# Optimization experiments

Measured on AMD Instinct MI355X. Metric: run time of the kernel, lower is better.

The kernel has to match this reference:

```python
import jax, jax.numpy as jnp
import numpy as np

B, H, W, D, C = 2, 16, 16, 16, 128
UNITS = 128
BN_EPS = 1e-3  # keras BatchNormalization default epsilon


def setup_inputs() -> dict:
    key = jax.random.key(0)
    ks = jax.random.split(key, 12)
    lim = np.sqrt(3.0 / C)  # VarianceScaling(1.0, fan_avg, uniform)
    inp = {
        "x": jax.random.normal(ks[0], (B, H, W, D, C), dtype=jnp.float32),
        "gamma": jnp.ones((C,), jnp.float32),
        "beta": jnp.zeros((C,), jnp.float32),
        "moving_mean": jax.random.normal(ks[1], (C,), jnp.float32) * 0.1,
        "moving_var": jnp.ones((C,), jnp.float32) + 0.1 * jax.random.uniform(ks[2], (C,)),
        "Wq": jax.random.uniform(ks[3], (C, UNITS), jnp.float32, -lim, lim),
        "bq": jnp.zeros((UNITS,), jnp.float32),
        "Wk": jax.random.uniform(ks[4], (C, UNITS), jnp.float32, -lim, lim),
        "bk": jnp.zeros((UNITS,), jnp.float32),
        "Wv": jax.random.uniform(ks[5], (C, UNITS), jnp.float32, -lim, lim),
        "bv": jnp.zeros((UNITS,), jnp.float32),
        # proj uses kernel_init(0.0) -> effectively ~0; use tiny scale to keep grads nonzero
        "Wp": jax.random.uniform(ks[6], (UNITS, UNITS), jnp.float32, -1e-5, 1e-5),
        "bp": jnp.zeros((UNITS,), jnp.float32),
    }
    return inp


def reference(x, gamma, beta, moving_mean, moving_var, Wq, bq, Wk, bk, Wv, bv, Wp, bp):
    # BatchNormalization (inference mode): per-channel affine normalization
    xn = (x - moving_mean) * jax.lax.rsqrt(moving_var + BN_EPS) * gamma + beta
    b, h, w, d, c = xn.shape
    n = h * w * d
    scale = jnp.asarray(UNITS, jnp.float32) ** -0.5
    q = (xn @ Wq + bq).reshape(b, n, UNITS)
    k = (xn @ Wk + bk).reshape(b, n, UNITS)
    v = (xn @ Wv + bv).reshape(b, n, UNITS)
    # full self-attention over flattened 3D spatial dims: [b, n, n] scores
    attn = jax.nn.softmax(jnp.einsum('bnc,bmc->bnm', q, k) * scale, axis=-1)
    proj = jnp.einsum('bnm,bmc->bnc', attn, v).reshape(b, h, w, d, UNITS)
    proj = proj @ Wp + bp
    return xn + proj
```

## Files before the change

kernel.cpp:

```cpp
#include <hip/hip_runtime.h>
#include <hip/hip_bf16.h>

using bh8     = __attribute__((ext_vector_type(8))) short;
using floatx4 = __attribute__((ext_vector_type(4))) float;
using uintx2  = __attribute__((ext_vector_type(2))) unsigned;

#define MFMA16 __builtin_amdgcn_mfma_f32_16x16x32_bf16

__device__ __forceinline__ float b2f(short s) {
    union { unsigned u; float f; } v; v.u = ((unsigned)(unsigned short)s) << 16; return v.f;
}
__device__ __forceinline__ short f2b(float f) {
    union { float f; unsigned u; } v; v.f = f;
    unsigned r = (v.u + 0x7fffu + ((v.u >> 16) & 1u)) >> 16;
    return (short)r;
}
__device__ __forceinline__ unsigned pk2(float a, float b) {
    union { __hip_bfloat162 h; unsigned u; } v;
    v.h = __float22bfloat162_rn(make_float2(a, b));
    return v.u;
}
__device__ __forceinline__ float ldf(const void* p, int i, bool f32) {
    return f32 ? ((const float*)p)[i] : b2f(((const short*)p)[i]);
}
__device__ __forceinline__ bool detect_f32(const void* gamma) {
    return ((*(const unsigned*)gamma) & 0xFFFFu) == 0u;
}
__device__ __forceinline__ void gl2lds16(const short* g, short* l) {
    __builtin_amdgcn_global_load_lds(
        (const __attribute__((address_space(1))) void*)g,
        (__attribute__((address_space(3))) void*)l, 16, 0, 0);
}

#define WAITV(N) do { asm volatile("s_waitcnt vmcnt(" #N ")" ::: "memory"); \
                      __builtin_amdgcn_sched_barrier(0); } while (0)

#define LDW 136

__global__ __launch_bounds__(256) void k_bn_qkv(
    const void* __restrict__ xp,
    const void* __restrict__ gp, const void* __restrict__ bep,
    const void* __restrict__ mmp, const void* __restrict__ mvp,
    const void* __restrict__ Wqp, const void* __restrict__ bqp,
    const void* __restrict__ Wkp, const void* __restrict__ bkp,
    const void* __restrict__ Wvp, const void* __restrict__ bvp,
    short* __restrict__ Qo, short* __restrict__ Ko, short* __restrict__ Vt)
{
    __shared__ float sS[128], sT[128];
    __shared__ __align__(16) short Wt[128 * LDW];
    const bool f32 = detect_f32(gp);
    const int tid = threadIdx.x, wave = tid >> 6, lane = tid & 63;
    const int lq = lane >> 4, lr = lane & 15;
    const int g = blockIdx.x >> 6;
    const int tile = blockIdx.x & 63;
    const int row0 = tile * 128 + wave * 32;

    if (tid < 128) {
        float ga = ldf(gp, tid, f32), be = ldf(bep, tid, f32);
        float mm = ldf(mmp, tid, f32), mv = ldf(mvp, tid, f32);
        float s = ga * rsqrtf(mv + 1e-3f);
        sS[tid] = s;
        sT[tid] = be - mm * s;
    }

    const void* W  = (g == 0) ? Wqp : ((g == 1) ? Wkp : Wvp);
    const void* bb = (g == 0) ? bqp : ((g == 1) ? bkp : bvp);

    if (f32) {
        for (int it = 0; it < 16; ++it) {
            int f = (it * 256 + tid) * 4;
            int c = f >> 7, u = f & 127;
            floatx4 wv = *(const floatx4*)((const float*)W + f);
            #pragma unroll
            for (int jj = 0; jj < 4; ++jj) {
                int j = (jj + (tid >> 1)) & 3;
                Wt[(u + j) * LDW + c] = f2b(wv[j]);
            }
        }
    } else {
        for (int it = 0; it < 8; ++it) {
            int f = (it * 256 + tid) * 8;
            int c = f >> 7, u = f & 127;
            bh8 wv = *(const bh8*)((const short*)W + f);
            #pragma unroll
            for (int jj = 0; jj < 8; ++jj) {
                int j = (jj + tid) & 7;
                Wt[(u + j) * LDW + c] = wv[j];
            }
        }
    }
    __syncthreads();

    bh8 a[2][4];
    #pragma unroll
    for (int rt = 0; rt < 2; ++rt)
        #pragma unroll
        for (int ks = 0; ks < 4; ++ks) {
            int c0 = ks * 32 + lq * 8;
            floatx4 s0 = *(const floatx4*)(&sS[c0]), s1 = *(const floatx4*)(&sS[c0 + 4]);
            floatx4 t0 = *(const floatx4*)(&sT[c0]), t1 = *(const floatx4*)(&sT[c0 + 4]);
            bh8 af;
            if (f32) {
                const float* xr = (const float*)xp + (size_t)(row0 + rt * 16 + lr) * 128 + c0;
                floatx4 x0 = *(const floatx4*)xr, x1 = *(const floatx4*)(xr + 4);
                #pragma unroll
                for (int j = 0; j < 4; ++j) {
                    af[j]     = f2b(x0[j] * s0[j] + t0[j]);
                    af[j + 4] = f2b(x1[j] * s1[j] + t1[j]);
                }
            } else {
                bh8 xv = *(const bh8*)((const short*)xp + (size_t)(row0 + rt * 16 + lr) * 128 + c0);
                #pragma unroll
                for (int j = 0; j < 4; ++j) {
                    af[j]     = f2b(b2f(xv[j]) * s0[j] + t0[j]);
                    af[j + 4] = f2b(b2f(xv[j + 4]) * s1[j] + t1[j]);
                }
            }
            a[rt][ks] = af;
        }

    floatx4 acc[2][8] = {};
    #pragma unroll
    for (int ks = 0; ks < 4; ++ks)
        #pragma unroll
        for (int t = 0; t < 8; ++t) {
            bh8 b = *(const bh8*)(&Wt[(t * 16 + lr) * LDW + ks * 32 + lq * 8]);
            #pragma unroll
            for (int rt = 0; rt < 2; ++rt)
                acc[rt][t] = MFMA16(a[rt][ks], b, acc[rt][t], 0, 0, 0);
        }

    if (g < 2) {
        #pragma unroll
        for (int t = 0; t < 8; ++t) {
            int u = t * 16 + lr;
            float bias = ldf(bb, u, f32);
            #pragma unroll
            for (int rt = 0; rt < 2; ++rt)
                #pragma unroll
                for (int r = 0; r < 4; ++r) {
                    int grow = row0 + rt * 16 + lq * 4 + r;
                    short vb = f2b(acc[rt][t][r] + bias);
                    if (g == 0) Qo[(size_t)grow * 128 + u] = vb;
                    else        Ko[(size_t)grow * 128 + u] = vb;
                }
        }
    } else {
        __syncthreads();
        short* sVt = Wt;
        #pragma unroll
        for (int t = 0; t < 8; ++t) {
            int u = t * 16 + lr;
            float bias = ldf(bb, u, f32);
            #pragma unroll
            for (int rt = 0; rt < 2; ++rt)
                #pragma unroll
                for (int r = 0; r < 4; ++r) {
                    int n = wave * 32 + rt * 16 + lq * 4 + r;
                    sVt[u * LDW + n] = f2b(acc[rt][t][r] + bias);
                }
        }
        __syncthreads();
        int u = tid >> 1, nh = tid & 1;
        int grow0 = tile * 128 + nh * 64;
        int bsb = grow0 >> 12, nn = grow0 & 4095;
        short* dst = Vt + (size_t)bsb * 128 * 4096 + (size_t)u * 4096 + nn;
        #pragma unroll
        for (int j = 0; j < 8; ++j)
            *(bh8*)(dst + j * 8) = *(const bh8*)(&sVt[u * LDW + nh * 64 + j * 8]);
    }
}

#define PLDA 40

__global__ __launch_bounds__(256, 2) void k_attn(
    const short* __restrict__ Qg, const short* __restrict__ Kg,
    const short* __restrict__ Vtg, short* __restrict__ Op,
    float* __restrict__ Lq)
{
    __shared__ __align__(16) short sK[4][32 * 128];
    __shared__ __align__(16) short sV[4][128 * 32];
    __shared__ __align__(16) short sP[4][32 * PLDA];

    const int tid = threadIdx.x, wave = tid >> 6, lane = tid & 63;
    const int lq = lane >> 4, lr = lane & 15;
    const int qt = blockIdx.x >> 3, kq = blockIdx.x & 7;
    const int mq = qt * 128, bs = mq >> 12, key0q = kq * 512;
    const short* Kb = Kg + (size_t)bs * 4096 * 128;
    const short* Vb = Vtg + (size_t)bs * 128 * 4096;
    const int qrow0 = mq + wave * 32;

    bh8 aq[2][4];
    #pragma unroll
    for (int rt = 0; rt < 2; ++rt)
        #pragma unroll
        for (int ks = 0; ks < 4; ++ks)
            aq[rt][ks] = *(const bh8*)(Qg + (size_t)(qrow0 + rt * 16 + lr) * 128 + ks * 32 + lq * 8);

    const int kKey = lane >> 4, kCh = lane & 15;
    const int vU   = lane >> 2, vCh = lane & 3;

    floatx4 accO[2][8] = {};
    float lsum[2] = {};
    const float c2 = 0.12751743f;
    const float m2 = 11.541560f;
    short* Pw = &sP[wave][0];

    auto stage = [&](int tt, int bb) {
        const int key1 = key0q + tt * 32;
        #pragma unroll
        for (int rd = 0; rd < 2; ++rd) {
            int key = wave * 8 + rd * 4 + kKey;
            gl2lds16(Kb + (size_t)(key1 + key) * 128 + ((kCh ^ (key & 7)) << 3),
                     &sK[bb][(wave * 8 + rd * 4) * 128]);
        }
        #pragma unroll
        for (int rd = 0; rd < 2; ++rd) {
            int u = wave * 32 + rd * 16 + vU;
            gl2lds16(Vb + (size_t)u * 4096 + key1 + ((vCh ^ ((u >> 1) & 3)) << 3),
                     &sV[bb][(wave * 32 + rd * 16) * 32]);
        }
    };

    auto do_tile = [&](int bb) {
        __builtin_amdgcn_s_barrier();
        __builtin_amdgcn_sched_barrier(0);
        const short* sKp = &sK[bb][0];
        const short* sVp = &sV[bb][0];

        floatx4 s[2][2];
        #pragma unroll
        for (int rt = 0; rt < 2; ++rt)
            #pragma unroll
            for (int t = 0; t < 2; ++t)
                s[rt][t] = floatx4{};
        #pragma unroll
        for (int t = 0; t < 2; ++t)
            #pragma unroll
            for (int ks = 0; ks < 4; ++ks) {
                bh8 kf = *(const bh8*)(&sKp[(t * 16 + lr) * 128 +
                                            (((ks * 4 + lq) ^ (lr & 7)) << 3)]);
                #pragma unroll
                for (int rt = 0; rt < 2; ++rt)
                    s[rt][t] = MFMA16(kf, aq[rt][ks], s[rt][t], 0, 0, 0);
            }

        #pragma unroll
        for (int rt = 0; rt < 2; ++rt)
            #pragma unroll
            for (int t = 0; t < 2; ++t) {
                float e[4];
                #pragma unroll
                for (int r = 0; r < 4; ++r) {
                    e[r] = exp2f(fmaf(s[rt][t][r], c2, -m2));
                    lsum[rt] += e[r];
                }
                uintx2 pw;
                pw[0] = pk2(e[0], e[1]);
                pw[1] = pk2(e[2], e[3]);
                *(uintx2*)(&Pw[(rt * 16 + lr) * PLDA + t * 16 + lq * 4]) = pw;
            }

        bh8 ap[2];
        #pragma unroll
        for (int rt = 0; rt < 2; ++rt)
            ap[rt] = *(const bh8*)(&Pw[(rt * 16 + lr) * PLDA + lq * 8]);

        #pragma unroll
        for (int t = 0; t < 8; ++t) {
            int u = t * 16 + lr;
            bh8 b = *(const bh8*)(&sVp[u * 32 + ((lq ^ ((lr >> 1) & 3)) << 3)]);
            #pragma unroll
            for (int rt = 0; rt < 2; ++rt)
                accO[rt][t] = MFMA16(ap[rt], b, accO[rt][t], 0, 0, 0);
        }
        __builtin_amdgcn_sched_barrier(0);
        __builtin_amdgcn_s_barrier();
    };

    stage(0, 0); stage(1, 1); stage(2, 2); stage(3, 3);

    #pragma unroll 4
    for (int t = 0; t < 12; ++t) {
        WAITV(12);
        do_tile(t & 3);
        stage(t + 4, t & 3);
    }
    WAITV(12); do_tile(0);
    WAITV(8);  do_tile(1);
    WAITV(4);  do_tile(2);
    WAITV(0);  do_tile(3);

    #pragma unroll
    for (int rt = 0; rt < 2; ++rt) {
        float v = lsum[rt];
        v += __shfl_xor(v, 16, 64);
        v += __shfl_xor(v, 32, 64);
        if (lane < 16)
            Lq[(size_t)kq * 8192 + qrow0 + rt * 16 + lr] = v;
    }
    short* Ob = Op + (size_t)kq * 8192 * 128;
    #pragma unroll
    for (int rt = 0; rt < 2; ++rt)
        #pragma unroll
        for (int t = 0; t < 8; ++t)
            #pragma unroll
            for (int r = 0; r < 4; ++r)
                Ob[(size_t)(qrow0 + rt * 16 + lq * 4 + r) * 128 + t * 16 + lr]
                    = f2b(accO[rt][t][r]);
}

__global__ __launch_bounds__(256, 2) void k_proj(
    const short* __restrict__ Op, const float* __restrict__ Lq,
    const void* __restrict__ Wpp, const void* __restrict__ bpp,
    const void* __restrict__ xp,
    const void* __restrict__ gp, const void* __restrict__ bep,
    const void* __restrict__ mmp, const void* __restrict__ mvp,
    void* __restrict__ outp)
{
    __shared__ float sS[128], sT[128];
    __shared__ __align__(16) short Wt[128 * LDW];
    __shared__ __align__(16) short sO[16 * LDW];
    const bool f32 = detect_f32(gp);
    const int tid = threadIdx.x, wave = tid >> 6, lane = tid & 63;
    const int lq = lane >> 4, lr = lane & 15;
    const int row0 = blockIdx.x * 16;

    if (tid < 128) {
        float ga = ldf(gp, tid, f32), be = ldf(bep, tid, f32);
        float mm = ldf(mmp, tid, f32), mv = ldf(mvp, tid, f32);
        float s = ga * rsqrtf(mv + 1e-3f);
        sS[tid] = s;
        sT[tid] = be - mm * s;
    }

    if (f32) {
        for (int it = 0; it < 16; ++it) {
            int f = (it * 256 + tid) * 4;
            int c = f >> 7, u = f & 127;
            floatx4 wv = *(const floatx4*)((const float*)Wpp + f);
            #pragma unroll
            for (int jj = 0; jj < 4; ++jj) {
                int j = (jj + (tid >> 1)) & 3;
                Wt[(u + j) * LDW + c] = f2b(wv[j]);
            }
        }
    } else {
        for (int it = 0; it < 8; ++it) {
            int f = (it * 256 + tid) * 8;
            int c = f >> 7, u = f & 127;
            bh8 wv = *(const bh8*)((const short*)Wpp + f);
            #pragma unroll
            for (int jj = 0; jj < 8; ++jj) {
                int j = (jj + tid) & 7;
                Wt[(u + j) * LDW + c] = wv[j];
            }
        }
    }

    {
        int f = tid * 8;
        int row = f >> 7, c = f & 127;
        int grow = row0 + row;
        float L = 0.f;
        #pragma unroll
        for (int w = 0; w < 8; ++w) L += Lq[(size_t)w * 8192 + grow];
        float invL = 1.0f / L;
        float sum[8] = {};
        #pragma unroll
        for (int w = 0; w < 8; ++w) {
            bh8 p = *(const bh8*)(Op + (size_t)w * 8192 * 128 + (size_t)grow * 128 + c);
            #pragma unroll
            for (int j = 0; j < 8; ++j) sum[j] += b2f(p[j]);
        }
        bh8 o;
        #pragma unroll
        for (int j = 0; j < 8; ++j) o[j] = f2b(sum[j] * invL);
        *(bh8*)(&sO[row * LDW + c]) = o;
    }
    __syncthreads();

    bh8 a[4];
    #pragma unroll
    for (int ks = 0; ks < 4; ++ks)
        a[ks] = *(const bh8*)(&sO[lr * LDW + ks * 32 + lq * 8]);

    floatx4 acc[2] = {};
    #pragma unroll
    for (int ks = 0; ks < 4; ++ks)
        #pragma unroll
        for (int tt = 0; tt < 2; ++tt) {
            bh8 b = *(const bh8*)(&Wt[(wave * 32 + tt * 16 + lr) * LDW + ks * 32 + lq * 8]);
            acc[tt] = MFMA16(a[ks], b, acc[tt], 0, 0, 0);
        }

    #pragma unroll
    for (int tt = 0; tt < 2; ++tt) {
        int u = wave * 32 + tt * 16 + lr;
        float bias = ldf(bpp, u, f32);
        float su = sS[u], tu = sT[u];
        #pragma unroll
        for (int r = 0; r < 4; ++r) {
            int grow = row0 + lq * 4 + r;
            float xnv = ldf(xp, grow * 128 + u, f32) * su + tu;
            float v = acc[tt][r] + bias + xnv;
            size_t idx = (size_t)grow * 128 + u;
            if (f32) ((float*)outp)[idx] = v;
            else     ((short*)outp)[idx] = f2b(v);
        }
    }
}

extern "C" void kernel_launch(void* const* d_in, const int* in_sizes, int n_in,
                              void* d_out, int out_size, void* d_ws, size_t ws_size,
                              hipStream_t stream)
{
    const void* x     = d_in[0];
    const void* gamma = d_in[1];
    const void* beta  = d_in[2];
    const void* mmean = d_in[3];
    const void* mvar  = d_in[4];
    const void* Wq    = d_in[5];
    const void* bq    = d_in[6];
    const void* Wk    = d_in[7];
    const void* bk    = d_in[8];
    const void* Wv    = d_in[9];
    const void* bv    = d_in[10];
    const void* Wp    = d_in[11];
    const void* bp    = d_in[12];

    char* ws = (char*)d_ws;
    const size_t MB = 1024u * 1024u;
    short* Q     = (short*)(ws + 0 * MB);
    short* K     = (short*)(ws + 2 * MB);
    short* Vt    = (short*)(ws + 4 * MB);
    short* Opart = (short*)(ws + 6 * MB);
    float* Lsum  = (float*)(ws + 22 * MB);

    k_bn_qkv<<<192, 256, 0, stream>>>(x, gamma, beta, mmean, mvar,
                                      Wq, bq, Wk, bk, Wv, bv, Q, K, Vt);
    k_attn<<<512, 256, 0, stream>>>(Q, K, Vt, Opart, Lsum);
    k_proj<<<512, 256, 0, stream>>>(Opart, Lsum, Wp, bp, x,
                                    gamma, beta, mmean, mvar, d_out);
}
```

Measured before the change: 129.4 us.

## Software-pipeline attention: overlap QK^T/softmax of next tile with PV of previous

```diff
diff --git a/kernel.cpp b/kernel.cpp
--- a/kernel.cpp
+++ b/kernel.cpp
@@ -178,9 +178,9 @@
     const short* __restrict__ Vtg, short* __restrict__ Op,
     float* __restrict__ Lq)
 {
-    __shared__ __align__(16) short sK[4][32 * 128];
-    __shared__ __align__(16) short sV[4][128 * 32];
-    __shared__ __align__(16) short sP[4][32 * PLDA];
+    __shared__ __align__(16) short sK[3][32 * 128];
+    __shared__ __align__(16) short sV[3][128 * 32];
+    __shared__ __align__(16) short sP[4][2][32 * PLDA];
 
     const int tid = threadIdx.x, wave = tid >> 6, lane = tid & 63;
     const int lq = lane >> 4, lr = lane & 15;
@@ -204,7 +204,6 @@
     float lsum[2] = {};
     const float c2 = 0.12751743f;
     const float m2 = 11.541560f;
-    short* Pw = &sP[wave][0];
 
     auto stage = [&](int tt, int bb) {
         const int key1 = key0q + tt * 32;
@@ -222,74 +221,90 @@
         }
     };
 
-    auto do_tile = [&](int bb) {
-        __builtin_amdgcn_s_barrier();
-        __builtin_amdgcn_sched_barrier(0);
+    auto qkt_sm = [&](int bb, int ss) {
         const short* sKp = &sK[bb][0];
-        const short* sVp = &sV[bb][0];
-
+        short* Pw = &sP[wave][ss][0];
         floatx4 s[2][2];
         #pragma unroll
         for (int rt = 0; rt < 2; ++rt)
             #pragma unroll
-            for (int t = 0; t < 2; ++t)
-                s[rt][t] = floatx4{};
-        #pragma unroll
-        for (int t = 0; t < 2; ++t)
+            for (int tt = 0; tt < 2; ++tt)
+                s[rt][tt] = floatx4{};
+        #pragma unroll
+        for (int tt = 0; tt < 2; ++tt)
             #pragma unroll
             for (int ks = 0; ks < 4; ++ks) {
-                bh8 kf = *(const bh8*)(&sKp[(t * 16 + lr) * 128 +
+                bh8 kf = *(const bh8*)(&sKp[(tt * 16 + lr) * 128 +
                                             (((ks * 4 + lq) ^ (lr & 7)) << 3)]);
                 #pragma unroll
                 for (int rt = 0; rt < 2; ++rt)
-                    s[rt][t] = MFMA16(kf, aq[rt][ks], s[rt][t], 0, 0, 0);
-            }
-
+                    s[rt][tt] = MFMA16(kf, aq[rt][ks], s[rt][tt], 0, 0, 0);
+            }
         #pragma unroll
         for (int rt = 0; rt < 2; ++rt)
             #pragma unroll
-            for (int t = 0; t < 2; ++t) {
+            for (int tt = 0; tt < 2; ++tt) {
                 float e[4];
                 #pragma unroll
                 for (int r = 0; r < 4; ++r) {
-                    e[r] = exp2f(fmaf(s[rt][t][r], c2, -m2));
+                    e[r] = exp2f(fmaf(s[rt][tt][r], c2, -m2));
                     lsum[rt] += e[r];
                 }
                 uintx2 pw;
                 pw[0] = pk2(e[0], e[1]);
                 pw[1] = pk2(e[2], e[3]);
-                *(uintx2*)(&Pw[(rt * 16 + lr) * PLDA + t * 16 + lq * 4]) = pw;
-            }
-
+                *(uintx2*)(&Pw[(rt * 16 + lr) * PLDA + tt * 16 + lq * 4]) = pw;
+            }
+    };
+
+    auto pv = [&](int bb, int ss) {
+        const short* sVp = &sV[bb][0];
+        const short* Pw = &sP[wave][ss][0];
         bh8 ap[2];
         #pragma unroll
         for (int rt = 0; rt < 2; ++rt)
             ap[rt] = *(const bh8*)(&Pw[(rt * 16 + lr) * PLDA + lq * 8]);
-
-        #pragma unroll
-        for (int t = 0; t < 8; ++t) {
-            int u = t * 16 + lr;
+        #pragma unroll
+        for (int tt = 0; tt < 8; ++tt) {
+            int u = tt * 16 + lr;
             bh8 b = *(const bh8*)(&sVp[u * 32 + ((lq ^ ((lr >> 1) & 3)) << 3)]);
             #pragma unroll
             for (int rt = 0; rt < 2; ++rt)
-                accO[rt][t] = MFMA16(ap[rt], b, accO[rt][t], 0, 0, 0);
-        }
-        __builtin_amdgcn_sched_barrier(0);
-        __builtin_amdgcn_s_barrier();
+                accO[rt][tt] = MFMA16(ap[rt], b, accO[rt][tt], 0, 0, 0);
+        }
     };
 
-    stage(0, 0); stage(1, 1); stage(2, 2); stage(3, 3);
-
-    #pragma unroll 4
-    for (int t = 0; t < 12; ++t) {
-        WAITV(12);
-        do_tile(t & 3);
-        stage(t + 4, t & 3);
-    }
-    WAITV(12); do_tile(0);
-    WAITV(8);  do_tile(1);
-    WAITV(4);  do_tile(2);
-    WAITV(0);  do_tile(3);
+    #define BAR() do { __builtin_amdgcn_sched_barrier(0); \
+                       __builtin_amdgcn_s_barrier(); \
+                       __builtin_amdgcn_sched_barrier(0); } while (0)
+
+    stage(0, 0); stage(1, 1);
+
+    WAITV(4); BAR();
+    qkt_sm(0, 0);
+    BAR();
+    stage(2, 2);
+
+    #pragma unroll
+    for (int t = 1; t <= 13; ++t) {
+        WAITV(4); BAR();
+        qkt_sm(t % 3, t & 1);
+        pv((t - 1) % 3, (t - 1) & 1);
+        BAR();
+        stage(t + 2, (t + 2) % 3);
+    }
+
+    WAITV(4); BAR();
+    qkt_sm(14 % 3, 0);
+    pv(13 % 3, 1);
+    BAR();
+    WAITV(0); BAR();
+    qkt_sm(15 % 3, 1);
+    pv(14 % 3, 0);
+    BAR();
+    pv(15 % 3, 1);
+
+    #undef BAR
 
     #pragma unroll
     for (int rt = 0; rt < 2; ++rt) {
```

Measured after the change: 140.4 us. +8.5%, slower.
